# Kernel tuning notes

Hardware: AMD Instinct MI355X
Metric: run time of the kernel (lower is better)

The kernel has to match this reference:

```python
import math
import jax, jax.numpy as jnp
import numpy as np

HEADS = 8
DIM_HEAD = 64
MAX_POS_EMB = 512


def setup_inputs() -> dict:
    key = jax.random.key(0)
    ks = jax.random.split(key, 6)
    dim = 512
    inner = HEADS * DIM_HEAD  # 512
    x = jax.random.normal(ks[0], (16, 3900, dim), jnp.float32)
    wq = jax.random.normal(ks[1], (dim, inner), jnp.float32) * 0.02
    wkv = jax.random.normal(ks[2], (dim, 2 * inner), jnp.float32) * 0.02
    wout_w = jax.random.normal(ks[3], (inner, dim), jnp.float32) * 0.02
    wout_b = jax.random.normal(ks[4], (dim,), jnp.float32) * 0.02
    rel_pos_table = jax.random.normal(ks[5], (2 * MAX_POS_EMB + 1, DIM_HEAD), jnp.float32) * 0.02
    return {"x": x, "wq": wq, "wkv": wkv, "wout_w": wout_w, "wout_b": wout_b,
            "rel_pos_table": rel_pos_table, "context_size": 200}


def reference(x, wq, wkv, wout_w, wout_b, rel_pos_table, context_size):
    bs, n, d = x.shape
    h, dh = HEADS, DIM_HEAD
    c = context_size
    scale = dh ** -0.5
    nb = math.ceil(n / c)
    nr = n % c
    if nr > 0:
        x = jnp.pad(x, ((0, 0), (0, c - nr), (0, 0)))  # [bs, nb*c, d]
    np_tok = nb * c
    q = x @ wq                     # [bs, np, inner]
    kv = x @ wkv                   # [bs, np, 2*inner]
    k, v = jnp.split(kv, 2, axis=-1)
    # [bs, nb, c, h, dh] -> [bs, nb, h, c, dh]
    def to_heads(t):
        return t.reshape(bs, nb, c, h, dh).transpose(0, 1, 3, 2, 4)
    q, k, v = to_heads(q), to_heads(k), to_heads(v)
    dots = jnp.einsum('bmhid,bmhjd->bmhij', q, k) * scale  # [bs, nb, h, c, c]
    # relative position bias (Transformer-XL style within chunk)
    seq = jnp.arange(c)
    dist = jnp.clip(seq[:, None] - seq[None, :], -c, c) + MAX_POS_EMB  # [c, c]
    rel = rel_pos_table[dist]  # [c, c, dh]
    pos_attn = jnp.einsum('bmhcd,crd->bmhcr', q, rel) * scale
    dots = dots + pos_attn
    if nr > 0:
        # last chunk: mask everything except the valid top-left nr x nr block
        mask = jnp.ones((c, c), dtype=bool).at[:nr, :nr].set(False)
        mask_value = -jnp.finfo(dots.dtype).max
        dots = dots.at[:, -1].set(jnp.where(mask, mask_value, dots[:, -1]))
    attn = jax.nn.softmax(dots, axis=-1)
    out = jnp.einsum('bmhij,bmhjd->bmhid', attn, v)  # [bs, nb, h, c, dh]
    out = out.transpose(0, 1, 3, 2, 4).reshape(bs, np_tok, h * dh)
    out = out[:, :n, :] @ wout_w + wout_b  # dropout is identity at eval
    return out
```

## Files before the change

kernel.cpp:

```cpp
#include <hip/hip_runtime.h>
#include <hip/hip_bf16.h>
#include <cstdint>
#include <cstddef>

#define BS 16
#define SEQ 3900
#define DIM 512
#define NHEAD 8
#define DH 64
#define CHUNK 200
#define NB 20
#define NR 100
#define NP 4000
#define MAXPOS 512
#define MD 62400

typedef __attribute__((ext_vector_type(8))) short bf16x8;
typedef __attribute__((ext_vector_type(8))) unsigned short u16x8;
typedef __attribute__((ext_vector_type(4))) float f32x4;
#define MFMA_BF16 __builtin_amdgcn_mfma_f32_16x16x32_bf16

static __device__ __forceinline__ float bf2f(unsigned short u) {
  union { unsigned int i; float f; } v; v.i = ((unsigned int)u) << 16; return v.f;
}
static __device__ __forceinline__ unsigned short f2bf(float f) {
  unsigned int x = __float_as_uint(f);
  unsigned int lsb = (x >> 16) & 1u;
  x += 0x7fffu + lsb;
  return (unsigned short)(x >> 16);
}

static __device__ __forceinline__ void gload16(const void* g, void* l) {
  auto gp = reinterpret_cast<const __attribute__((address_space(1))) unsigned int*>(
      reinterpret_cast<uintptr_t>(g));
  auto lp = reinterpret_cast<__attribute__((address_space(3))) unsigned int*>(
      reinterpret_cast<uintptr_t>(l));
  __builtin_amdgcn_global_load_lds(gp, lp, 16, 0, 0);
}

static __device__ __forceinline__ const unsigned short* wt_row(
    const unsigned short* base, int n) {
  unsigned ch = (unsigned)n / 100u;
  unsigned rr = (unsigned)n - ch * 100u;
  return base + (size_t)ch * (NP * DIM) + (size_t)SEQ * DIM + (size_t)rr * DIM;
}

__global__ __launch_bounds__(256) void prep_table(
    const float* __restrict__ table, unsigned short* __restrict__ Tb)
{
  int idx = (blockIdx.x * 256 + threadIdx.x) * 4;
  if (idx < 416 * 64) {
    float4 f = *reinterpret_cast<const float4*>(table + (size_t)305 * 64 + idx);
    ushort4 o;
    o.x = f2bf(f.x); o.y = f2bf(f.y); o.z = f2bf(f.z); o.w = f2bf(f.w);
    *reinterpret_cast<ushort4*>(Tb + idx) = o;
  }
}

__global__ __launch_bounds__(256) void wtrans(
    const float* __restrict__ W, int ldn, int n_off, float scale,
    unsigned short* __restrict__ base)
{
  __shared__ float ts[64][65];
  const int tid = threadIdx.x;
  const int n0 = blockIdx.x * 64;
  const int k0 = blockIdx.y * 64;
  {
    int kl = tid >> 4;
    int nl = (tid & 15) * 4;
#pragma unroll
    for (int p = 0; p < 4; ++p) {
      float4 f = *reinterpret_cast<const float4*>(
          W + (size_t)(k0 + kl + p * 16) * ldn + n0 + nl);
      ts[kl + p * 16][nl + 0] = f.x;
      ts[kl + p * 16][nl + 1] = f.y;
      ts[kl + p * 16][nl + 2] = f.z;
      ts[kl + p * 16][nl + 3] = f.w;
    }
  }
  __syncthreads();
  {
    int nl = tid >> 2;
    int kof = (tid & 3) * 16;
    int n = n0 + nl + n_off;
    unsigned ch = (unsigned)n / 100u;
    unsigned rr = (unsigned)n - ch * 100u;
    unsigned short* dst = base + (size_t)ch * (NP * DIM) + (size_t)SEQ * DIM
                          + (size_t)rr * DIM + k0 + kof;
    u16x8 o0, o1;
#pragma unroll
    for (int i = 0; i < 8; ++i) o0[i] = f2bf(ts[kof + i][nl] * scale);
#pragma unroll
    for (int i = 0; i < 8; ++i) o1[i] = f2bf(ts[kof + 8 + i][nl] * scale);
    *reinterpret_cast<u16x8*>(dst) = o0;
    *reinterpret_cast<u16x8*>(dst + 8) = o1;
  }
}

__global__ __launch_bounds__(256) void cast_x(
    const float* __restrict__ x, unsigned short* __restrict__ xb)
{
  const size_t total = (size_t)MD * DIM;
  size_t i = ((size_t)blockIdx.x * 256 + threadIdx.x) * 8;
  const size_t stride = (size_t)gridDim.x * 256 * 8;
  for (; i < total; i += stride) {
    float4 f0 = *reinterpret_cast<const float4*>(x + i);
    float4 f1 = *reinterpret_cast<const float4*>(x + i + 4);
    u16x8 o;
    o[0] = f2bf(f0.x); o[1] = f2bf(f0.y); o[2] = f2bf(f0.z); o[3] = f2bf(f0.w);
    o[4] = f2bf(f1.x); o[5] = f2bf(f1.y); o[6] = f2bf(f1.z); o[7] = f2bf(f1.w);
    *reinterpret_cast<u16x8*>(xb + i) = o;
  }
}

__global__ __launch_bounds__(256) void gemm_qkv(
    const unsigned short* __restrict__ xb, const unsigned short* __restrict__ WtBase,
    unsigned short* __restrict__ Qb, unsigned short* __restrict__ Kb,
    unsigned short* __restrict__ Vb)
{
  __shared__ unsigned short LDS[4][8 * 512];

  int bid = blockIdx.x;
  bid = (bid & 7) * 732 + (bid >> 3);
  const int bm = bid / 12, bn = bid % 12;
  const int m0 = bm * 128, n0 = bn * 128;
  const int tid = threadIdx.x;
  const int wv = tid >> 6, ln = tid & 63;
  const int wr = wv >> 1, wc = wv & 1;
  const int lr = ln & 15, lg = ln >> 4;

  const int sl = ln & 15, sk = (ln >> 4) * 8;
  const int q0 = wv * 2, q1 = q0 + 1;
  int ar0 = m0 + (q0 >> 2) * 64 + (q0 & 3) * 16 + sl; if (ar0 >= MD) ar0 = MD - 1;
  int ar1 = m0 + (q1 >> 2) * 64 + (q1 & 3) * 16 + sl; if (ar1 >= MD) ar1 = MD - 1;
  const unsigned short* aS0 = xb + (size_t)ar0 * DIM + sk;
  const unsigned short* aS1 = xb + (size_t)ar1 * DIM + sk;
  const unsigned short* bS0 = wt_row(WtBase, n0 + (q0 >> 2) * 64 + (q0 & 3) * 16 + sl) + sk;
  const unsigned short* bS1 = wt_row(WtBase, n0 + (q1 >> 2) * 64 + (q1 & 3) * 16 + sl) + sk;

  f32x4 acc[4][4];
#pragma unroll
  for (int i = 0; i < 4; ++i)
#pragma unroll
    for (int j = 0; j < 4; ++j) acc[i][j] = (f32x4){0.f, 0.f, 0.f, 0.f};

#define STG_QKV(buf, koff)                            \
  gload16(aS0 + (koff), &LDS[buf][q0 * 512]);         \
  gload16(aS1 + (koff), &LDS[buf][q1 * 512]);         \
  gload16(bS0 + (koff), &LDS[2 + buf][q0 * 512]);     \
  gload16(bS1 + (koff), &LDS[2 + buf][q1 * 512]);

  STG_QKV(0, 0)
  __syncthreads();

  int p = 0;
  for (int s = 0; s < 16; ++s) {
    if (s < 15) { STG_QKV(p ^ 1, (s + 1) * 32) }
    const unsigned short* asp = LDS[p];
    const unsigned short* bsp = LDS[2 + p];
    bf16x8 af[4], bfr[4];
#pragma unroll
    for (int mt = 0; mt < 4; ++mt)
      af[mt] = *reinterpret_cast<const bf16x8*>(asp + (wr * 4 + mt) * 512 + ln * 8);
#pragma unroll
    for (int nt = 0; nt < 4; ++nt)
      bfr[nt] = *reinterpret_cast<const bf16x8*>(bsp + (wc * 4 + nt) * 512 + ln * 8);
#pragma unroll
    for (int mt = 0; mt < 4; ++mt)
#pragma unroll
      for (int nt = 0; nt < 4; ++nt)
        acc[mt][nt] = MFMA_BF16(af[mt], bfr[nt], acc[mt][nt], 0, 0, 0);
    __syncthreads();
    p ^= 1;
  }

  unsigned short* dst; int nbase;
  if (n0 < 512)       { dst = Qb; nbase = 0; }
  else if (n0 < 1024) { dst = Kb; nbase = 512; }
  else                { dst = Vb; nbase = 1024; }
  const int dcol0 = n0 - nbase;

  unsigned char* Cb8 = reinterpret_cast<unsigned char*>(&LDS[0][0]);
#pragma unroll
  for (int mt = 0; mt < 4; ++mt) {
#pragma unroll
    for (int e = 0; e < 4; ++e) {
      int r = wr * 64 + mt * 16 + lg * 4 + e;
#pragma unroll
      for (int nt = 0; nt < 4; ++nt) {
        int c2 = (wc * 128 + nt * 32 + lr * 2) ^ (lg << 5);
        *reinterpret_cast<unsigned short*>(Cb8 + r * 256 + c2) = f2bf(acc[mt][nt][e]);
      }
    }
  }
  __syncthreads();
  {
    const int g = tid >> 4, l16 = tid & 15;
#pragma unroll
    for (int i = 0; i < 8; ++i) {
      int r = g * 8 + i;
      int off = (l16 * 16) ^ (((r >> 2) & 3) << 5);
      uint4 v = *reinterpret_cast<const uint4*>(Cb8 + r * 256 + off);
      unsigned rd = m0 + r;
      if (rd < MD) {
        unsigned bb = rd / 3900u;
        unsigned tt = rd - bb * 3900u;
        *reinterpret_cast<uint4*>(dst + ((size_t)bb * NP + tt) * DIM + dcol0 + l16 * 8) = v;
      }
    }
  }
}

__global__ __launch_bounds__(256) void gemm_out(
    const unsigned short* __restrict__ Ob, const unsigned short* __restrict__ WoBase,
    const float* __restrict__ bias, float* __restrict__ out)
{
  __shared__ unsigned short LDS[4][8 * 512];

  int bid = blockIdx.x;
  bid = (bid & 7) * 244 + (bid >> 3);
  const int bm = bid / 4, bn = bid % 4;
  const int m0 = bm * 128, n0 = bn * 128;
  const int tid = threadIdx.x;
  const int wv = tid >> 6, ln = tid & 63;
  const int wr = wv >> 1, wc = wv & 1;
  const int lr = ln & 15, lg = ln >> 4;

  const int sl = ln & 15, sk = (ln >> 4) * 8;
  const int q0 = wv * 2, q1 = q0 + 1;
  unsigned ar0 = m0 + (q0 >> 2) * 64 + (q0 & 3) * 16 + sl; if (ar0 >= MD) ar0 = MD - 1;
  unsigned ar1 = m0 + (q1 >> 2) * 64 + (q1 & 3) * 16 + sl; if (ar1 >= MD) ar1 = MD - 1;
  unsigned b0b = ar0 / 3900u, t0 = ar0 - b0b * 3900u;
  unsigned b1b = ar1 / 3900u, t1 = ar1 - b1b * 3900u;
  const unsigned short* aS0 = Ob + ((size_t)b0b * NP + t0) * DIM + sk;
  const unsigned short* aS1 = Ob + ((size_t)b1b * NP + t1) * DIM + sk;
  const unsigned short* bS0 = wt_row(WoBase, n0 + (q0 >> 2) * 64 + (q0 & 3) * 16 + sl) + sk;
  const unsigned short* bS1 = wt_row(WoBase, n0 + (q1 >> 2) * 64 + (q1 & 3) * 16 + sl) + sk;

  f32x4 acc[4][4];
#pragma unroll
  for (int i = 0; i < 4; ++i)
#pragma unroll
    for (int j = 0; j < 4; ++j) acc[i][j] = (f32x4){0.f, 0.f, 0.f, 0.f};

#define STG_OUT(buf, koff)                            \
  gload16(aS0 + (koff), &LDS[buf][q0 * 512]);         \
  gload16(aS1 + (koff), &LDS[buf][q1 * 512]);         \
  gload16(bS0 + (koff), &LDS[2 + buf][q0 * 512]);     \
  gload16(bS1 + (koff), &LDS[2 + buf][q1 * 512]);

  STG_OUT(0, 0)
  __syncthreads();

  int p = 0;
  for (int s = 0; s < 16; ++s) {
    if (s < 15) { STG_OUT(p ^ 1, (s + 1) * 32) }
    const unsigned short* asp = LDS[p];
    const unsigned short* bsp = LDS[2 + p];
    bf16x8 af[4], bfr[4];
#pragma unroll
    for (int mt = 0; mt < 4; ++mt)
      af[mt] = *reinterpret_cast<const bf16x8*>(asp + (wr * 4 + mt) * 512 + ln * 8);
#pragma unroll
    for (int nt = 0; nt < 4; ++nt)
      bfr[nt] = *reinterpret_cast<const bf16x8*>(bsp + (wc * 4 + nt) * 512 + ln * 8);
#pragma unroll
    for (int mt = 0; mt < 4; ++mt)
#pragma unroll
      for (int nt = 0; nt < 4; ++nt)
        acc[mt][nt] = MFMA_BF16(af[mt], bfr[nt], acc[mt][nt], 0, 0, 0);
    __syncthreads();
    p ^= 1;
  }

  char* Cf = reinterpret_cast<char*>(&LDS[0][0]);
  const int gg = tid >> 5, l32 = tid & 31;
#pragma unroll
  for (int pass = 0; pass < 2; ++pass) {
    if (wr == pass) {
#pragma unroll
      for (int mt = 0; mt < 4; ++mt)
#pragma unroll
        for (int e = 0; e < 4; ++e) {
          int rl = mt * 16 + lg * 4 + e;
#pragma unroll
          for (int nt = 0; nt < 4; ++nt) {
            int c4 = (wc * 256 + nt * 64 + lr * 4) ^ (lg << 6);
            *reinterpret_cast<float*>(Cf + rl * 512 + c4) = acc[mt][nt][e];
          }
        }
    }
    __syncthreads();
#pragma unroll
    for (int i = 0; i < 8; ++i) {
      int rl = gg * 8 + i;
      int off = (l32 * 16) ^ (((rl >> 2) & 3) << 6);
      float4 v = *reinterpret_cast<const float4*>(Cf + rl * 512 + off);
      int c = l32 * 4;
      float4 bv4 = *reinterpret_cast<const float4*>(bias + n0 + c);
      v.x += bv4.x; v.y += bv4.y; v.z += bv4.z; v.w += bv4.w;
      unsigned rd = m0 + pass * 64 + rl;
      if (rd < MD)
        *reinterpret_cast<float4*>(out + (size_t)rd * DIM + n0 + c) = v;
    }
    if (pass == 0) __syncthreads();
  }
}

#define KS_U16 12800
#define VT_U16 13568
#define PQ_STR 228
#define PQ_U16 (16*PQ_STR)
#define ATTN_LDS_B ((KS_U16 + VT_U16 + 4*PQ_U16) * 2)

__global__ __launch_bounds__(256) void attn_mfma(
    const unsigned short* __restrict__ Qb, const unsigned short* __restrict__ Kb,
    const unsigned short* __restrict__ Vb, const unsigned short* __restrict__ Tb,
    unsigned short* __restrict__ Ob)
{
  extern __shared__ unsigned short smem[];
  unsigned short* Ks = smem;
  unsigned short* Vt = smem + KS_U16;

  const int tid = threadIdx.x;
  const int bid = blockIdx.x;
  const int h  = bid & 7;
  const int bm = bid >> 3;
  const int m  = bm % NB;
  const int b  = bm / NB;
  const size_t rowbase = (size_t)b * NP + (size_t)m * CHUNK;
  const int lim = (m == NB - 1) ? NR : CHUNK;

  for (int c = tid; c < CHUNK * 8; c += 256) {
    int j = c >> 3, k0 = (c & 7) * 8;
    uint4 kv = *reinterpret_cast<const uint4*>(Kb + (rowbase + j) * DIM + h * DH + k0);
    int byte = (j * 128 + k0 * 2) ^ ((j & 7) << 4);
    *reinterpret_cast<uint4*>(reinterpret_cast<char*>(Ks) + byte) = kv;
    uint4 vv4 = *reinterpret_cast<const uint4*>(Vb + (rowbase + j) * DIM + h * DH + k0);
    const unsigned short* vs = reinterpret_cast<const unsigned short*>(&vv4);
#pragma unroll
    for (int e = 0; e < 8; ++e)
      Vt[(k0 + e) * 212 + j] = vs[e];
  }
  __syncthreads();

  const int wv = tid >> 6, ln = tid & 63;
  const int lr = ln & 15, lg = ln >> 4;
  unsigned short* pq = smem + KS_U16 + VT_U16 + wv * PQ_U16;

  const int nMt = (lim + 15) >> 4;
  for (int mt = wv; mt < nMt; mt += 4) {
    const int i0 = mt << 4;

    const unsigned short* qp = Qb + (rowbase + i0 + lr) * DIM + h * DH + lg * 8;
    bf16x8 qa0 = *reinterpret_cast<const bf16x8*>(qp);
    bf16x8 qa1 = *reinterpret_cast<const bf16x8*>(qp + 32);

#pragma unroll
    for (int ct = 0; ct < 14; ++ct) {
      const unsigned short* tp = Tb + (size_t)(i0 + ct * 16 + lr) * 64 + lg * 8;
      bf16x8 tb0 = *reinterpret_cast<const bf16x8*>(tp);
      bf16x8 tb1 = *reinterpret_cast<const bf16x8*>(tp + 32);
      f32x4 acc = {0.f, 0.f, 0.f, 0.f};
      acc = MFMA_BF16(qa0, tb0, acc, 0, 0, 0);
      acc = MFMA_BF16(qa1, tb1, acc, 0, 0, 0);
#pragma unroll
      for (int e = 0; e < 4; ++e)
        pq[(lg * 4 + e) * PQ_STR + ct * 16 + lr] = f2bf(acc[e]);
    }

    f32x4 s[13];
#pragma unroll
    for (int nt = 0; nt < 13; ++nt) {
      int row = nt * 16 + lr;
      int b0 = (row * 128 + lg * 16) ^ ((row & 7) << 4);
      int b1 = (row * 128 + 64 + lg * 16) ^ ((row & 7) << 4);
      bf16x8 k0 = *reinterpret_cast<const bf16x8*>(reinterpret_cast<char*>(Ks) + b0);
      bf16x8 k1 = *reinterpret_cast<const bf16x8*>(reinterpret_cast<char*>(Ks) + b1);
      f32x4 acc = {0.f, 0.f, 0.f, 0.f};
      acc = MFMA_BF16(qa0, k0, acc, 0, 0, 0);
      acc = MFMA_BF16(qa1, k1, acc, 0, 0, 0);
      s[nt] = acc;
    }

    float sv[4] = {0.f, 0.f, 0.f, 0.f};
#pragma unroll
    for (int nt = 0; nt < 13; ++nt) {
      int j = nt * 16 + lr;
#pragma unroll
      for (int e = 0; e < 4; ++e) {
        int r = lg * 4 + e;
        float pos = bf2f(pq[r * PQ_STR + (r - j + 207)]);
        float t = s[nt][e] + pos;
        float p = (j < lim) ? exp2f(t) : 0.f;
        s[nt][e] = p;
        sv[e] += p;
      }
    }
#pragma unroll
    for (int e = 0; e < 4; ++e) {
      float x = sv[e];
      x += __shfl_xor(x, 1);
      x += __shfl_xor(x, 2);
      x += __shfl_xor(x, 4);
      x += __shfl_xor(x, 8);
      sv[e] = __builtin_amdgcn_rcpf(x);
    }

#pragma unroll
    for (int nt = 0; nt < 13; ++nt)
#pragma unroll
      for (int e = 0; e < 4; ++e)
        pq[(lg * 4 + e) * PQ_STR + nt * 16 + lr] = f2bf(s[nt][e]);

    f32x4 o[4];
#pragma unroll
    for (int nt = 0; nt < 4; ++nt) o[nt] = (f32x4){0.f, 0.f, 0.f, 0.f};
    const ushort4 zz = {0, 0, 0, 0};
#pragma unroll
    for (int ks = 0; ks < 7; ++ks) {
      union __align__(16) { struct { ushort4 lo, hi; } u; bf16x8 v; } pa;
      if (ks < 6 || lg < 2) {
        const char* pap = reinterpret_cast<const char*>(pq) + lr * (PQ_STR * 2) + ks * 64 + lg * 16;
        pa.u.lo = *reinterpret_cast<const ushort4*>(pap);
        pa.u.hi = *reinterpret_cast<const ushort4*>(pap + 8);
      } else {
        pa.u.lo = zz; pa.u.hi = zz;
      }
#pragma unroll
      for (int nt = 0; nt < 4; ++nt) {
        union __align__(16) { struct { ushort4 lo, hi; } u; bf16x8 v; } vb;
        if (ks < 6 || lg == 0) {
          const char* vbp = reinterpret_cast<const char*>(Vt) + (nt * 16 + lr) * 424 + ks * 64 + lg * 16;
          vb.u.lo = *reinterpret_cast<const ushort4*>(vbp);
          vb.u.hi = *reinterpret_cast<const ushort4*>(vbp + 8);
        } else {
          vb.u.lo = zz; vb.u.hi = zz;
        }
        o[nt] = MFMA_BF16(pa.v, vb.v, o[nt], 0, 0, 0);
      }
    }

#pragma unroll
    for (int nt = 0; nt < 4; ++nt)
#pragma unroll
      for (int e = 0; e < 4; ++e) {
        int i = i0 + lg * 4 + e;
        if (i < lim) {
          Ob[(rowbase + i) * DIM + h * DH + nt * 16 + lr] = f2bf(o[nt][e] * sv[e]);
        }
      }
  }
}

extern "C" void kernel_launch(void* const* d_in, const int* in_sizes, int n_in,
                              void* d_out, int out_size, void* d_ws, size_t ws_size,
                              hipStream_t stream) {
  const float* x   = (const float*)d_in[0];
  const float* wq  = (const float*)d_in[1];
  const float* wkv = (const float*)d_in[2];
  const float* wo  = (const float*)d_in[3];
  const float* wb  = (const float*)d_in[4];
  const float* tbl = (const float*)d_in[5];
  float* out = (float*)d_out;

  const size_t elems = (size_t)BS * NP * DIM;
  unsigned short* Qb = (unsigned short*)d_ws;
  unsigned short* Kb = Qb + elems;
  unsigned short* Vb = Kb + elems;
  unsigned short* Ob = Qb;
  unsigned short* Tb = Kb + (size_t)SEQ * DIM;
  unsigned short* xb = (unsigned short*)d_out;

  hipFuncSetAttribute(reinterpret_cast<const void*>(attn_mfma),
                      hipFuncAttributeMaxDynamicSharedMemorySize, ATTN_LDS_B);

  const float qscale = 0.125f * 1.44269504088896f;
  dim3 blk(256);
  prep_table<<<dim3(26), blk, 0, stream>>>(tbl, Tb);
  wtrans<<<dim3(8, 8),  blk, 0, stream>>>(wq,  512,  0,   qscale, Qb);
  wtrans<<<dim3(16, 8), blk, 0, stream>>>(wkv, 1024, 512, 1.0f,   Qb);
  wtrans<<<dim3(8, 8),  blk, 0, stream>>>(wo,  512,  0,   1.0f,   Vb);
  cast_x<<<dim3(2048), blk, 0, stream>>>(x, xb);
  gemm_qkv<<<dim3(5856), blk, 0, stream>>>(xb, Qb, Qb, Kb, Vb);
  attn_mfma<<<dim3(BS * NB * NHEAD), blk, ATTN_LDS_B, stream>>>(Qb, Kb, Vb, Tb, Ob);
  gemm_out<<<dim3(1952), blk, 0, stream>>>(Ob, Vb, wb, out);
}
```

Measured before the change: 501.8 us.

## Merge prep kernels into one launch and enlarge QKV GEMM tile to 256x128

```diff
diff --git a/kernel.cpp b/kernel.cpp
--- a/kernel.cpp
+++ b/kernel.cpp
@@ -45,26 +45,14 @@
   return base + (size_t)ch * (NP * DIM) + (size_t)SEQ * DIM + (size_t)rr * DIM;
 }
 
-__global__ __launch_bounds__(256) void prep_table(
-    const float* __restrict__ table, unsigned short* __restrict__ Tb)
-{
-  int idx = (blockIdx.x * 256 + threadIdx.x) * 4;
-  if (idx < 416 * 64) {
-    float4 f = *reinterpret_cast<const float4*>(table + (size_t)305 * 64 + idx);
-    ushort4 o;
-    o.x = f2bf(f.x); o.y = f2bf(f.y); o.z = f2bf(f.z); o.w = f2bf(f.w);
-    *reinterpret_cast<ushort4*>(Tb + idx) = o;
-  }
-}
-
-__global__ __launch_bounds__(256) void wtrans(
+static __device__ void wtrans_body(
     const float* __restrict__ W, int ldn, int n_off, float scale,
-    unsigned short* __restrict__ base)
+    unsigned short* __restrict__ base, int nb, int kb)
 {
   __shared__ float ts[64][65];
   const int tid = threadIdx.x;
-  const int n0 = blockIdx.x * 64;
-  const int k0 = blockIdx.y * 64;
+  const int n0 = nb * 64;
+  const int k0 = kb * 64;
   {
     int kl = tid >> 4;
     int nl = (tid & 15) * 4;
@@ -97,12 +85,38 @@
   }
 }
 
-__global__ __launch_bounds__(256) void cast_x(
-    const float* __restrict__ x, unsigned short* __restrict__ xb)
+#define CAST_BLOCKS 2048
+#define PREP_BLOCKS (64 + 128 + 64 + 26 + CAST_BLOCKS)
+
+__global__ __launch_bounds__(256) void prep_all(
+    const float* __restrict__ x, const float* __restrict__ wq,
+    const float* __restrict__ wkv, const float* __restrict__ wo,
+    const float* __restrict__ tbl,
+    unsigned short* __restrict__ Qb, unsigned short* __restrict__ Vb,
+    unsigned short* __restrict__ Tb, unsigned short* __restrict__ xb,
+    float qscale)
 {
+  int bid = blockIdx.x;
+  if (bid < 64) { wtrans_body(wq, 512, 0, qscale, Qb, bid & 7, bid >> 3); return; }
+  bid -= 64;
+  if (bid < 128) { wtrans_body(wkv, 1024, 512, 1.0f, Qb, bid & 15, bid >> 4); return; }
+  bid -= 128;
+  if (bid < 64) { wtrans_body(wo, 512, 0, 1.0f, Vb, bid & 7, bid >> 3); return; }
+  bid -= 64;
+  if (bid < 26) {
+    int idx = (bid * 256 + threadIdx.x) * 4;
+    if (idx < 416 * 64) {
+      float4 f = *reinterpret_cast<const float4*>(tbl + (size_t)305 * 64 + idx);
+      ushort4 o;
+      o.x = f2bf(f.x); o.y = f2bf(f.y); o.z = f2bf(f.z); o.w = f2bf(f.w);
+      *reinterpret_cast<ushort4*>(Tb + idx) = o;
+    }
+    return;
+  }
+  bid -= 26;
   const size_t total = (size_t)MD * DIM;
-  size_t i = ((size_t)blockIdx.x * 256 + threadIdx.x) * 8;
-  const size_t stride = (size_t)gridDim.x * 256 * 8;
+  size_t i = ((size_t)bid * 256 + threadIdx.x) * 8;
+  const size_t stride = (size_t)CAST_BLOCKS * 256 * 8;
   for (; i < total; i += stride) {
     float4 f0 = *reinterpret_cast<const float4*>(x + i);
     float4 f1 = *reinterpret_cast<const float4*>(x + i + 4);
@@ -113,30 +127,35 @@
   }
 }
 
-__global__ __launch_bounds__(256) void gemm_qkv(
+__global__ __launch_bounds__(512) void gemm_qkv(
     const unsigned short* __restrict__ xb, const unsigned short* __restrict__ WtBase,
     unsigned short* __restrict__ Qb, unsigned short* __restrict__ Kb,
     unsigned short* __restrict__ Vb)
 {
-  __shared__ unsigned short LDS[4][8 * 512];
+  __shared__ unsigned short LDS[2][24 * 512];
 
   int bid = blockIdx.x;
-  bid = (bid & 7) * 732 + (bid >> 3);
+  bid = (bid & 7) * 366 + (bid >> 3);
   const int bm = bid / 12, bn = bid % 12;
-  const int m0 = bm * 128, n0 = bn * 128;
+  const int m0 = bm * 256, n0 = bn * 128;
   const int tid = threadIdx.x;
   const int wv = tid >> 6, ln = tid & 63;
   const int wr = wv >> 1, wc = wv & 1;
   const int lr = ln & 15, lg = ln >> 4;
 
   const int sl = ln & 15, sk = (ln >> 4) * 8;
-  const int q0 = wv * 2, q1 = q0 + 1;
-  int ar0 = m0 + (q0 >> 2) * 64 + (q0 & 3) * 16 + sl; if (ar0 >= MD) ar0 = MD - 1;
-  int ar1 = m0 + (q1 >> 2) * 64 + (q1 & 3) * 16 + sl; if (ar1 >= MD) ar1 = MD - 1;
-  const unsigned short* aS0 = xb + (size_t)ar0 * DIM + sk;
-  const unsigned short* aS1 = xb + (size_t)ar1 * DIM + sk;
-  const unsigned short* bS0 = wt_row(WtBase, n0 + (q0 >> 2) * 64 + (q0 & 3) * 16 + sl) + sk;
-  const unsigned short* bS1 = wt_row(WtBase, n0 + (q1 >> 2) * 64 + (q1 & 3) * 16 + sl) + sk;
+  const unsigned short* src[3];
+#pragma unroll
+  for (int t = 0; t < 3; ++t) {
+    int sb = wv * 3 + t;
+    if (sb < 16) {
+      int ar = m0 + sb * 16 + sl; if (ar >= MD) ar = MD - 1;
+      src[t] = xb + (size_t)ar * DIM + sk;
+    } else {
+      src[t] = wt_row(WtBase, n0 + (sb - 16) * 16 + sl) + sk;
+    }
+  }
+  const int dst0 = (wv * 3) * 512;
 
   f32x4 acc[4][4];
 #pragma unroll
@@ -144,27 +163,25 @@
 #pragma unroll
     for (int j = 0; j < 4; ++j) acc[i][j] = (f32x4){0.f, 0.f, 0.f, 0.f};
 
-#define STG_QKV(buf, koff)                            \
-  gload16(aS0 + (koff), &LDS[buf][q0 * 512]);         \
-  gload16(aS1 + (koff), &LDS[buf][q1 * 512]);         \
-  gload16(bS0 + (koff), &LDS[2 + buf][q0 * 512]);     \
-  gload16(bS1 + (koff), &LDS[2 + buf][q1 * 512]);
-
-  STG_QKV(0, 0)
+#define STG256(buf, koff)                              \
+  gload16(src[0] + (koff), &LDS[buf][dst0]);           \
+  gload16(src[1] + (koff), &LDS[buf][dst0 + 512]);     \
+  gload16(src[2] + (koff), &LDS[buf][dst0 + 1024]);
+
+  STG256(0, 0)
   __syncthreads();
 
   int p = 0;
   for (int s = 0; s < 16; ++s) {
-    if (s < 15) { STG_QKV(p ^ 1, (s + 1) * 32) }
-    const unsigned short* asp = LDS[p];
-    const unsigned short* bsp = LDS[2 + p];
+    if (s < 15) { STG256(p ^ 1, (s + 1) * 32) }
+    const unsigned short* lsp = LDS[p];
     bf16x8 af[4], bfr[4];
 #pragma unroll
     for (int mt = 0; mt < 4; ++mt)
-      af[mt] = *reinterpret_cast<const bf16x8*>(asp + (wr * 4 + mt) * 512 + ln * 8);
+      af[mt] = *reinterpret_cast<const bf16x8*>(lsp + (wr * 4 + mt) * 512 + ln * 8);
 #pragma unroll
     for (int nt = 0; nt < 4; ++nt)
-      bfr[nt] = *reinterpret_cast<const bf16x8*>(bsp + (wc * 4 + nt) * 512 + ln * 8);
+      bfr[nt] = *reinterpret_cast<const bf16x8*>(lsp + (16 + wc * 4 + nt) * 512 + ln * 8);
 #pragma unroll
     for (int mt = 0; mt < 4; ++mt)
 #pragma unroll
@@ -182,32 +199,38 @@
 
   unsigned char* Cb8 = reinterpret_cast<unsigned char*>(&LDS[0][0]);
 #pragma unroll
-  for (int mt = 0; mt < 4; ++mt) {
-#pragma unroll
-    for (int e = 0; e < 4; ++e) {
-      int r = wr * 64 + mt * 16 + lg * 4 + e;
-#pragma unroll
-      for (int nt = 0; nt < 4; ++nt) {
-        int c2 = (wc * 128 + nt * 32 + lr * 2) ^ (lg << 5);
-        *reinterpret_cast<unsigned short*>(Cb8 + r * 256 + c2) = f2bf(acc[mt][nt][e]);
+  for (int pass = 0; pass < 2; ++pass) {
+    if ((wr >> 1) == pass) {
+#pragma unroll
+      for (int mt = 0; mt < 4; ++mt) {
+#pragma unroll
+        for (int e = 0; e < 4; ++e) {
+          int r = (wr & 1) * 64 + mt * 16 + lg * 4 + e;
+#pragma unroll
+          for (int nt = 0; nt < 4; ++nt) {
+            int c2 = (wc * 128 + nt * 32 + lr * 2) ^ (lg << 5);
+            *reinterpret_cast<unsigned short*>(Cb8 + r * 256 + c2) = f2bf(acc[mt][nt][e]);
+          }
+        }
       }
     }
-  }
-  __syncthreads();
-  {
-    const int g = tid >> 4, l16 = tid & 15;
-#pragma unroll
-    for (int i = 0; i < 8; ++i) {
-      int r = g * 8 + i;
-      int off = (l16 * 16) ^ (((r >> 2) & 3) << 5);
-      uint4 v = *reinterpret_cast<const uint4*>(Cb8 + r * 256 + off);
-      unsigned rd = m0 + r;
-      if (rd < MD) {
-        unsigned bb = rd / 3900u;
-        unsigned tt = rd - bb * 3900u;
-        *reinterpret_cast<uint4*>(dst + ((size_t)bb * NP + tt) * DIM + dcol0 + l16 * 8) = v;
+    __syncthreads();
+    {
+      const int g = tid >> 4, l16 = tid & 15;
+#pragma unroll
+      for (int i = 0; i < 4; ++i) {
+        int r = g * 4 + i;
+        int off = (l16 * 16) ^ (((r >> 2) & 3) << 5);
+        uint4 v = *reinterpret_cast<const uint4*>(Cb8 + r * 256 + off);
+        unsigned rd = m0 + pass * 128 + r;
+        if (rd < MD) {
+          unsigned bb = rd / 3900u;
+          unsigned tt = rd - bb * 3900u;
+          *reinterpret_cast<uint4*>(dst + ((size_t)bb * NP + tt) * DIM + dcol0 + l16 * 8) = v;
+        }
       }
     }
+    if (pass == 0) __syncthreads();
   }
 }
 
@@ -476,13 +499,9 @@
                       hipFuncAttributeMaxDynamicSharedMemorySize, ATTN_LDS_B);
 
   const float qscale = 0.125f * 1.44269504088896f;
-  dim3 blk(256);
-  prep_table<<<dim3(26), blk, 0, stream>>>(tbl, Tb);
-  wtrans<<<dim3(8, 8),  blk, 0, stream>>>(wq,  512,  0,   qscale, Qb);
-  wtrans<<<dim3(16, 8), blk, 0, stream>>>(wkv, 1024, 512, 1.0f,   Qb);
-  wtrans<<<dim3(8, 8),  blk, 0, stream>>>(wo,  512,  0,   1.0f,   Vb);
-  cast_x<<<dim3(2048), blk, 0, stream>>>(x, xb);
-  gemm_qkv<<<dim3(5856), blk, 0, stream>>>(xb, Qb, Qb, Kb, Vb);
-  attn_mfma<<<dim3(BS * NB * NHEAD), blk, ATTN_LDS_B, stream>>>(Qb, Kb, Vb, Tb, Ob);
-  gemm_out<<<dim3(1952), blk, 0, stream>>>(Ob, Vb, wb, out);
-}
+  prep_all<<<dim3(PREP_BLOCKS), dim3(256), 0, stream>>>(
+      x, wq, wkv, wo, tbl, Qb, Vb, Tb, xb, qscale);
+  gemm_qkv<<<dim3(2928), dim3(512), 0, stream>>>(xb, Qb, Qb, Kb, Vb);
+  attn_mfma<<<dim3(BS * NB * NHEAD), dim3(256), ATTN_LDS_B, stream>>>(Qb, Kb, Vb, Tb, Ob);
+  gemm_out<<<dim3(1952), dim3(256), 0, stream>>>(Ob, Vb, wb, out);
+}
```

New measurement: 508.9 us. Within noise of the previous version (+1.4%).
